# Kernel tuning notes

Measured on AMD Instinct MI355X. Metric: run time of the kernel, lower is better.

Reference implementation:

```python
import jax, jax.numpy as jnp
import numpy as np

LMAX = 2; C = 64; H = 8; D = C // H
N_NODES = 10000; N_EDGES = 160000
M = (LMAX + 1) ** 2                      # 9 spherical components
RAD_IN = 64; RAD_HID = 64
WNUM = (LMAX + 1) * C                    # per-edge CP-TP weights: one per (l, channel)
L_OF_M = jnp.array([l for l in range(LMAX + 1) for _ in range(2 * l + 1)])
LN_EPS = 1e-5


def _lin(x, W, b=None):
    # Linear over channel (last) dim; bias applied ONLY to scalar (m=0) component
    y = jnp.einsum('nmc,cd->nmd', x, W)
    if b is not None:
        y = y.at[:, 0, :].add(b)
    return y


def _cp_tp(x, sh, w_lc):
    # CP tensor product with SH: channelwise product, per-(l, channel) radial weight
    # x: [E, M, C], sh: [E, M], w_lc: [E, LMAX+1, C]
    return x * sh[:, :, None] * w_lc[:, L_OF_M, :]


def _radial(s, W1, b1, g, b, W2, off):
    h = s @ W1 + b1
    mu = h.mean(-1, keepdims=True)
    var = h.var(-1, keepdims=True)
    h = (h - mu) / jnp.sqrt(var + LN_EPS) * g + b
    h = jax.nn.silu(h)
    return (h @ W2 + off).reshape(-1, LMAX + 1, C)


def _smooth_lrelu(x, a=0.2):
    return (1 + a) / 2 * x + (1 - a) / 2 * x * (2 * jax.nn.sigmoid(x) - 1)


def _gate(x):
    c = x.shape[-1] // 2
    v = x[..., :c]
    g = jax.nn.sigmoid(x[:, 0, c:])[:, None, :]
    return jnp.concatenate([jax.nn.silu(v[:, :1, :]), v[:, 1:, :] * g], axis=1)


def _seg_softmax(a, idx, n):
    # numerically stable softmax over edges grouped by destination node
    m = jax.ops.segment_max(a, idx, num_segments=n)
    e = jnp.exp(a - m[idx])
    s = jax.ops.segment_sum(e, idx, num_segments=n)
    return e / (s[idx] + 1e-16)


def setup_inputs():
    key = jax.random.key(0)
    ks = jax.random.split(key, 16)
    def w(k, shape, fan_in):
        return jax.random.normal(k, shape, jnp.float32) / np.sqrt(fan_in)
    bound = 1.0 / np.sqrt(RAD_HID)
    return {
        'node_input': jax.random.normal(ks[0], (N_NODES, M, C), jnp.float32),
        'edge_attr': jax.random.normal(ks[1], (N_EDGES, M), jnp.float32),
        'edge_scalars': jax.random.normal(ks[2], (N_EDGES, RAD_IN), jnp.float32),
        'W_src': w(ks[3], (C, C), C), 'b_src': jnp.zeros((C,), jnp.float32),
        'W_dst': w(ks[4], (C, C), C),
        'rad_W1': w(ks[5], (RAD_IN, RAD_HID), RAD_IN),
        'rad_b1': jnp.zeros((RAD_HID,), jnp.float32),
        'rad_ln_g': jnp.ones((RAD_HID,), jnp.float32),
        'rad_ln_b': jnp.zeros((RAD_HID,), jnp.float32),
        'rad_W2': w(ks[6], (RAD_HID, WNUM), RAD_HID),
        'rad_offset': jax.random.uniform(ks[7], (WNUM,), jnp.float32, -bound, bound),
        'W_alpha': w(ks[8], (C, C), C), 'b_alpha': jnp.zeros((C,), jnp.float32),
        'alpha_dot': w(ks[9], (H, D), D),
        'W_value': w(ks[10], (C, 2 * C), C), 'b_value': jnp.zeros((2 * C,), jnp.float32),
        'W_proj': w(ks[11], (C, C), C), 'b_proj': jnp.zeros((C,), jnp.float32),
        'edge_src': jax.random.randint(ks[12], (N_EDGES,), 0, N_NODES),
        'edge_dst': jax.random.randint(ks[13], (N_EDGES,), 0, N_NODES),
        'batch': jnp.zeros((N_NODES,), jnp.int32),
    }


def reference(node_input, edge_attr, edge_scalars, W_src, b_src, W_dst,
              rad_W1, rad_b1, rad_ln_g, rad_ln_b, rad_W2, rad_offset,
              W_alpha, b_alpha, alpha_dot, W_value, b_value, W_proj, b_proj,
              edge_src, edge_dst, batch):
    # gather: per-edge merged message [E, M, C]
    msg = _lin(node_input, W_src, b_src)[edge_src] + _lin(node_input, W_dst)[edge_dst]
    # per-edge radial weights for both tensor products [E, LMAX+1, C]
    w_lc = _radial(edge_scalars, rad_W1, rad_b1, rad_ln_g, rad_ln_b, rad_W2, rad_offset)
    msg = _cp_tp(msg, edge_attr, w_lc)
    # alpha path: scalar channel only
    alpha = _lin(msg, W_alpha, b_alpha)[:, 0, :].reshape(-1, H, D)
    alpha = _smooth_lrelu(alpha)[:, None]                 # [E, 1, H, D]
    alpha = jnp.einsum('bikd,kd->bik', alpha, alpha_dot)  # [E, 1, H]
    alpha = _seg_softmax(alpha, edge_dst, N_NODES)        # dropout disabled (eval)
    # value path
    value = _gate(_lin(msg, W_value, b_value))
    value = _cp_tp(value, edge_attr, w_lc)
    value = value.reshape(N_EDGES, M, H, D)
    # scatter-aggregate to destination nodes
    out = jax.ops.segment_sum(value * alpha[:, :, :, None], edge_dst, num_segments=N_NODES)
    return _lin(out.reshape(N_NODES, M, C), W_proj, b_proj)
```

## Files before the change

kernel.cpp:

```cpp
#include <hip/hip_runtime.h>
#include <stdint.h>

#define NN 10000
#define NE 160000

struct BF16 { unsigned short v; };
typedef _Float16 h2_t __attribute__((ext_vector_type(2)));
typedef _Float16 f16x8 __attribute__((ext_vector_type(8)));
typedef float f32x4 __attribute__((ext_vector_type(4)));

__device__ __forceinline__ float cvt(float x) { return x; }
__device__ __forceinline__ float cvt(BF16 x) {
    union { unsigned int i; float f; } u; u.i = ((unsigned int)x.v) << 16; return u.f;
}
__device__ __forceinline__ unsigned short f2b_us(float f) {
    union { float f; unsigned int i; } v; v.f = f;
    unsigned int x = v.i;
    unsigned int lsb = (x >> 16) & 1u;
    x += 0x7fffu + lsb;
    return (unsigned short)(x >> 16);
}
__device__ __forceinline__ float rlane(float v, int l) {
    return __uint_as_float((unsigned int)__builtin_amdgcn_readlane(__float_as_uint(v), l));
}
__device__ __forceinline__ h2_t rlane_pk(h2_t v, int l) {
    union { h2_t h; unsigned int u; } c; c.h = v;
    c.u = (unsigned int)__builtin_amdgcn_readlane(c.u, l);
    return c.h;
}
__device__ __forceinline__ h2_t pkh2(float a, float b) {
    h2_t r; r[0] = (_Float16)a; r[1] = (_Float16)b; return r;
}
__device__ __forceinline__ float fdot2f(h2_t a, h2_t b, float c) {
#if __has_builtin(__builtin_amdgcn_fdot2)
    return __builtin_amdgcn_fdot2(a, b, c, false);
#else
    return fmaf((float)a[0], (float)b[0], fmaf((float)a[1], (float)b[1], c));
#endif
}
__device__ __forceinline__ float sigm(float x) { return 1.0f / (1.0f + __expf(-x)); }
__device__ __forceinline__ int clampi(int v, int hi) { return (unsigned)v >= (unsigned)hi ? 0 : v; }

__device__ __forceinline__ void stOut(float* p, size_t i, float v) { p[i] = v; }
__device__ __forceinline__ void stOut(unsigned short* p, size_t i, float v) { p[i] = f2b_us(v); }

__device__ __forceinline__ unsigned okey(float f) {
    unsigned b = __float_as_uint(f);
    return (b & 0x80000000u) ? ~b : (b | 0x80000000u);
}
__device__ __forceinline__ float okdec(unsigned k) {
    unsigned b = (k & 0x80000000u) ? (k ^ 0x80000000u) : ~k;
    return __uint_as_float(b);
}

__device__ __forceinline__ f16x8 ld8f16(const BF16* p) {
    uint4 v = *(const uint4*)p;
    unsigned w0 = v.x, w1 = v.y, w2 = v.z, w3 = v.w;
    f16x8 r;
    union { unsigned u; float f; } c;
    c.u = (w0 & 0xFFFFu) << 16;  r[0] = (_Float16)c.f;
    c.u = (w0 & 0xFFFF0000u);    r[1] = (_Float16)c.f;
    c.u = (w1 & 0xFFFFu) << 16;  r[2] = (_Float16)c.f;
    c.u = (w1 & 0xFFFF0000u);    r[3] = (_Float16)c.f;
    c.u = (w2 & 0xFFFFu) << 16;  r[4] = (_Float16)c.f;
    c.u = (w2 & 0xFFFF0000u);    r[5] = (_Float16)c.f;
    c.u = (w3 & 0xFFFFu) << 16;  r[6] = (_Float16)c.f;
    c.u = (w3 & 0xFFFF0000u);    r[7] = (_Float16)c.f;
    return r;
}
__device__ __forceinline__ f16x8 ld8f16(const float* p) {
    float4 a = *(const float4*)p;
    float4 b = *(const float4*)(p + 4);
    f16x8 r;
    r[0] = (_Float16)a.x; r[1] = (_Float16)a.y; r[2] = (_Float16)a.z; r[3] = (_Float16)a.w;
    r[4] = (_Float16)b.x; r[5] = (_Float16)b.y; r[6] = (_Float16)b.z; r[7] = (_Float16)b.w;
    return r;
}

__global__ void k0_zero(int* __restrict__ cnt, int* __restrict__ csr, int* __restrict__ flag,
                        float* __restrict__ nsum, unsigned* __restrict__ mseg,
                        float* __restrict__ sseg) {
    int i = blockIdx.x * blockDim.x + threadIdx.x;
    if (i == 0) *flag = 1;
    if (i < NN) cnt[i] = 0;
    if (i < NE) csr[i] = 0;
    if (i < NN * 8) { mseg[i] = 0u; sseg[i] = 0.f; }
    for (int j = i; j < NN * 576; j += gridDim.x * blockDim.x) nsum[j] = 0.f;
}

__global__ void kprobe(const unsigned short* __restrict__ x, int* __restrict__ flag) {
    int bad = 0;
    for (int i = threadIdx.x; i < 16384; i += blockDim.x) {
        unsigned e = (x[i] >> 7) & 0xFFu;
        bad += (e == 0xFFu);
    }
    if (bad > 0) atomicExch(flag, 0);
}

template<typename T>
__device__ void k1_body(const T* x, const T* Ws, const T* bs, const T* Wd,
                        _Float16* fs, _Float16* fd)
{
    int lane = threadIdx.x & 63;
    int wv = threadIdx.x >> 6;
    float ws[64], wd[64];
#pragma unroll
    for (int i = 0; i < 64; i++) { ws[i] = cvt(Ws[i * 64 + lane]); wd[i] = cvt(Wd[i * 64 + lane]); }
    float bsl = cvt(bs[lane]);
    const int ROWS = NN * 9;
    for (int r = blockIdx.x * 4 + wv; r < ROWS; r += gridDim.x * 4) {
        float xv = cvt(x[(size_t)r * 64 + lane]);
        float a0 = 0, a1 = 0, a2 = 0, a3 = 0, d0 = 0, d1 = 0, d2 = 0, d3 = 0;
#pragma unroll
        for (int i = 0; i < 64; i += 4) {
            float x0 = rlane(xv, i), x1 = rlane(xv, i + 1), x2 = rlane(xv, i + 2), x3 = rlane(xv, i + 3);
            a0 = fmaf(x0, ws[i], a0);     a1 = fmaf(x1, ws[i + 1], a1);
            a2 = fmaf(x2, ws[i + 2], a2); a3 = fmaf(x3, ws[i + 3], a3);
            d0 = fmaf(x0, wd[i], d0);     d1 = fmaf(x1, wd[i + 1], d1);
            d2 = fmaf(x2, wd[i + 2], d2); d3 = fmaf(x3, wd[i + 3], d3);
        }
        float as = a0 + a1 + a2 + a3;
        if ((r % 9) == 0) as += bsl;
        fs[(size_t)r * 64 + lane] = (_Float16)as;
        fd[(size_t)r * 64 + lane] = (_Float16)(d0 + d1 + d2 + d3);
    }
}

__global__ __launch_bounds__(256) void k1_feats(
    const void* x, const void* Ws, const void* bs, const void* Wd,
    _Float16* fs, _Float16* fd, const int* flag)
{
    if (*flag) k1_body((const BF16*)x, (const BF16*)Ws, (const BF16*)bs, (const BF16*)Wd, fs, fd);
    else       k1_body((const float*)x, (const float*)Ws, (const float*)bs, (const float*)Wd, fs, fd);
}

__global__ void k2a_count(const int* __restrict__ dst, int* __restrict__ cnt) {
    for (int e = blockIdx.x * blockDim.x + threadIdx.x; e < NE; e += gridDim.x * blockDim.x)
        atomicAdd(&cnt[clampi(dst[e], NN)], 1);
}

__global__ __launch_bounds__(1024) void k2b_scan(const int* __restrict__ cnt,
                                                 int* __restrict__ off, int* __restrict__ cur) {
    __shared__ int part[1024];
    int t = threadIdx.x;
    int base = t * 10;
    int loc[10]; int s = 0;
#pragma unroll
    for (int k = 0; k < 10; k++) { int i = base + k; int v = (i < NN) ? cnt[i] : 0; loc[k] = v; s += v; }
    part[t] = s; __syncthreads();
    for (int o = 1; o < 1024; o <<= 1) {
        int v = (t >= o) ? part[t - o] : 0;
        __syncthreads();
        part[t] += v;
        __syncthreads();
    }
    int run = (t == 0) ? 0 : part[t - 1];
#pragma unroll
    for (int k = 0; k < 10; k++) {
        int i = base + k;
        if (i < NN) { off[i] = run; cur[i] = run; run += loc[k]; }
    }
    if (t == 1023) off[NN] = part[1023];
}

__global__ void k2c_fill(const int* __restrict__ dst, int* __restrict__ cur, int* __restrict__ csr) {
    for (int e = blockIdx.x * blockDim.x + threadIdx.x; e < NE; e += gridDim.x * blockDim.x) {
        int d = clampi(dst[e], NN);
        int p = atomicAdd(&cur[d], 1);
        if ((unsigned)p < (unsigned)NE) csr[p] = e;
    }
}

template<typename T>
__device__ void k3m_body(const T* es, const T* W1, const T* b1g, const T* gg, const T* bbv,
                         const T* W2, const T* roff, _Float16* wlc,
                         _Float16 (*Yt)[200])
{
    const int lane = threadIdx.x & 63;
    const int c16 = lane & 15;
    const int kg  = lane >> 4;

    f16x8 bW1[4][2], bW2[12][2];
#pragma unroll
    for (int t = 0; t < 4; t++)
#pragma unroll
        for (int kh = 0; kh < 2; kh++) {
            f16x8 f;
#pragma unroll
            for (int j = 0; j < 8; j++) {
                int k = kh * 32 + kg * 8 + j;
                f[j] = (_Float16)cvt(W1[(size_t)k * 64 + t * 16 + c16]);
            }
            bW1[t][kh] = f;
        }
#pragma unroll
    for (int t = 0; t < 12; t++)
#pragma unroll
        for (int kh = 0; kh < 2; kh++) {
            f16x8 f;
#pragma unroll
            for (int j = 0; j < 8; j++) {
                int k = kh * 32 + kg * 8 + j;
                f[j] = (_Float16)cvt(W2[(size_t)k * 192 + t * 16 + c16]);
            }
            bW2[t][kh] = f;
        }
    float b1v[4], gv[4], bv[4], rv[12];
#pragma unroll
    for (int t = 0; t < 4; t++) {
        b1v[t] = cvt(b1g[t * 16 + c16]);
        gv[t]  = cvt(gg[t * 16 + c16]);
        bv[t]  = cvt(bbv[t * 16 + c16]);
    }
#pragma unroll
    for (int t = 0; t < 12; t++) rv[t] = cvt(roff[t * 16 + c16]);

    const int NT = NE / 16;
    for (int tile = blockIdx.x * 4 + (threadIdx.x >> 6); tile < NT; tile += gridDim.x * 4) {
        const int e0 = tile * 16;
        f16x8 a0 = ld8f16(&es[(size_t)(e0 + c16) * 64 + kg * 8]);
        f16x8 a1 = ld8f16(&es[(size_t)(e0 + c16) * 64 + 32 + kg * 8]);
        f32x4 h[4] = {{0,0,0,0},{0,0,0,0},{0,0,0,0},{0,0,0,0}};
#pragma unroll
        for (int t = 0; t < 4; t++) {
            h[t] = __builtin_amdgcn_mfma_f32_16x16x32_f16(a0, bW1[t][0], h[t], 0, 0, 0);
            h[t] = __builtin_amdgcn_mfma_f32_16x16x32_f16(a1, bW1[t][1], h[t], 0, 0, 0);
        }
#pragma unroll
        for (int r = 0; r < 4; r++) {
            float x0 = h[0][r] + b1v[0], x1 = h[1][r] + b1v[1];
            float x2 = h[2][r] + b1v[2], x3 = h[3][r] + b1v[3];
            float s = x0 + x1 + x2 + x3;
            float q = x0 * x0 + x1 * x1 + x2 * x2 + x3 * x3;
            s += __shfl_xor(s, 1, 64); q += __shfl_xor(q, 1, 64);
            s += __shfl_xor(s, 2, 64); q += __shfl_xor(q, 2, 64);
            s += __shfl_xor(s, 4, 64); q += __shfl_xor(q, 4, 64);
            s += __shfl_xor(s, 8, 64); q += __shfl_xor(q, 8, 64);
            float mu = s * (1.0f / 64.0f);
            float var = fmaxf(q * (1.0f / 64.0f) - mu * mu, 0.0f);
            float rs = rsqrtf(var + 1e-5f);
            int row = kg * 4 + r;
#pragma unroll
            for (int t = 0; t < 4; t++) {
                float xt = (t == 0) ? x0 : (t == 1) ? x1 : (t == 2) ? x2 : x3;
                float v = (xt - mu) * rs * gv[t] + bv[t];
                v = v * sigm(v);
                Yt[row][t * 16 + c16] = (_Float16)v;
            }
        }
        f16x8 a20 = *(const f16x8*)&Yt[c16][kg * 8];
        f16x8 a21 = *(const f16x8*)&Yt[c16][32 + kg * 8];
        f32x4 y[12] = {{0,0,0,0},{0,0,0,0},{0,0,0,0},{0,0,0,0},{0,0,0,0},{0,0,0,0},
                       {0,0,0,0},{0,0,0,0},{0,0,0,0},{0,0,0,0},{0,0,0,0},{0,0,0,0}};
#pragma unroll
        for (int t = 0; t < 12; t++) {
            y[t] = __builtin_amdgcn_mfma_f32_16x16x32_f16(a20, bW2[t][0], y[t], 0, 0, 0);
            y[t] = __builtin_amdgcn_mfma_f32_16x16x32_f16(a21, bW2[t][1], y[t], 0, 0, 0);
        }
#pragma unroll
        for (int t = 0; t < 12; t++)
#pragma unroll
            for (int r = 0; r < 4; r++)
                Yt[kg * 4 + r][t * 16 + c16] = (_Float16)(y[t][r] + rv[t]);
#pragma unroll
        for (int j = 0; j < 6; j++) {
            int c = lane + 64 * j;
            int row = c / 24;
            int cc = (c % 24) * 8;
            *(f16x8*)&wlc[(size_t)(e0 + row) * 192 + cc] = *(const f16x8*)&Yt[row][cc];
        }
    }
}

__global__ __launch_bounds__(256) void k3m_wlc(
    const void* es, const void* W1, const void* b1, const void* g, const void* bln,
    const void* W2, const void* roff, _Float16* wlc, const int* flag)
{
    __shared__ _Float16 Y[4][16][200];
    const int wv = threadIdx.x >> 6;
    if (*flag) k3m_body<BF16>((const BF16*)es, (const BF16*)W1, (const BF16*)b1, (const BF16*)g,
                              (const BF16*)bln, (const BF16*)W2, (const BF16*)roff, wlc, Y[wv]);
    else       k3m_body<float>((const float*)es, (const float*)W1, (const float*)b1, (const float*)g,
                               (const float*)bln, (const float*)W2, (const float*)roff, wlc, Y[wv]);
}

template<typename T>
__device__ void k4_body(const T* ea, const _Float16* fs, const _Float16* fd,
                        const _Float16* wlc, const T* Wa, const T* ba, const T* adot,
                        const int* esrc, const int* edst, float* alpha, unsigned* mseg)
{
    int lane = threadIdx.x & 63;
    int wv = threadIdx.x >> 6;
    int j2 = (lane & 31) * 2;
    h2_t wap[32];
#pragma unroll
    for (int i = 0; i < 32; i++)
        wap[i] = pkh2(cvt(Wa[(2 * i) * 64 + lane]), cvt(Wa[(2 * i + 1) * 64 + lane]));
    float bal = cvt(ba[lane]), adl = cvt(adot[lane]);
    for (int e = blockIdx.x * 4 + wv; e < NE; e += gridDim.x * 4) {
        int sn = clampi(esrc[e], NN), dn = clampi(edst[e], NN);
        h2_t fsp = *(const h2_t*)&fs[(size_t)sn * 576 + j2];
        h2_t fdp = *(const h2_t*)&fd[(size_t)dn * 576 + j2];
        h2_t wlp = *(const h2_t*)&wlc[(size_t)e * 192 + j2];
        float ea0 = cvt(ea[(size_t)e * 9]);
        float m0a = ((float)fsp[0] + (float)fdp[0]) * ea0 * (float)wlp[0];
        float m0b = ((float)fsp[1] + (float)fdp[1]) * ea0 * (float)wlp[1];
        h2_t m0p = pkh2(m0a, m0b);
        float a0 = bal, a1 = 0, a2 = 0, a3 = 0;
#pragma unroll
        for (int i = 0; i < 32; i += 4) {
            a0 = fdot2f(rlane_pk(m0p, i),     wap[i],     a0);
            a1 = fdot2f(rlane_pk(m0p, i + 1), wap[i + 1], a1);
            a2 = fdot2f(rlane_pk(m0p, i + 2), wap[i + 2], a2);
            a3 = fdot2f(rlane_pk(m0p, i + 3), wap[i + 3], a3);
        }
        float aw = a0 + a1 + a2 + a3;
        float f = aw * (0.2f + 0.8f * sigm(aw));
        float p = f * adl;
        p += __shfl_xor(p, 1, 64);
        p += __shfl_xor(p, 2, 64);
        p += __shfl_xor(p, 4, 64);
        if ((lane & 7) == 0) {
            alpha[(size_t)e * 8 + (lane >> 3)] = p;
            atomicMax(&mseg[dn * 8 + (lane >> 3)], okey(p));
        }
    }
}

__global__ __launch_bounds__(256) void k4_alpha(
    const void* ea, const _Float16* fs, const _Float16* fd, const _Float16* wlc,
    const void* Wa, const void* ba, const void* adot,
    const int* esrc, const int* edst, float* alpha, unsigned* mseg, const int* flag)
{
    if (*flag) k4_body((const BF16*)ea, fs, fd, wlc, (const BF16*)Wa, (const BF16*)ba,
                       (const BF16*)adot, esrc, edst, alpha, mseg);
    else       k4_body((const float*)ea, fs, fd, wlc, (const float*)Wa, (const float*)ba,
                       (const float*)adot, esrc, edst, alpha, mseg);
}

__global__ void k5b_expsum(const int* __restrict__ edst, const unsigned* __restrict__ mseg,
                           float* __restrict__ alpha, float* __restrict__ sseg) {
    int t = blockIdx.x * blockDim.x + threadIdx.x;
    if (t >= NE * 8) return;
    int e = t >> 3, h = t & 7;
    int dn = clampi(edst[e], NN);
    float m = okdec(mseg[dn * 8 + h]);
    float ex = __expf(alpha[t] - m);
    alpha[t] = ex;
    unsafeAtomicAdd(&sseg[dn * 8 + h], ex);
}

template<typename T>
__device__ void k6m_body(const int* off, const int* csr, const int* esrc,
                         const T* ea, const _Float16* fs, const _Float16* fd,
                         const _Float16* wlc, const T* Wv, const T* bv,
                         const float* alpha, const float* sseg, float* nsum,
                         _Float16 (*wlS)[16][72], float (*mtS)[20])
{
    const int lane = threadIdx.x & 63;
    const int wvid = threadIdx.x >> 6;
    const int c16 = lane & 15;
    const int kg  = lane >> 4;

    for (int gw = blockIdx.x * 4 + wvid; gw < NN * 2; gw += gridDim.x * 4) {
        const int n = gw >> 1;
        const int half = gw & 1;
        const int b = off[n], e_end = off[n + 1];
        if (b >= e_end) continue;

        f16x8 bfV[2][2], bfG[2][2];
        float bvv[2], bgv[2];
        int colg[2], hh[2];
        float invs[2];
#pragma unroll
        for (int t = 0; t < 2; t++) {
            colg[t] = (half * 2 + t) * 16 + c16;
            hh[t] = colg[t] >> 3;
            invs[t] = 1.0f / (sseg[n * 8 + hh[t]] + 1e-16f);
#pragma unroll
            for (int kh = 0; kh < 2; kh++) {
                f16x8 b8v, b8g;
#pragma unroll
                for (int j = 0; j < 8; j++) {
                    int k = kh * 32 + kg * 8 + j;
                    b8v[j] = (_Float16)cvt(Wv[(size_t)k * 128 + colg[t]]);
                    b8g[j] = (_Float16)cvt(Wv[(size_t)k * 128 + 64 + colg[t]]);
                }
                bfV[t][kh] = b8v; bfG[t][kh] = b8g;
            }
            bvv[t] = cvt(bv[colg[t]]);
            bgv[t] = cvt(bv[64 + colg[t]]);
        }

        const size_t fdb = (size_t)n * 576;
        const size_t nbase = (size_t)n * 576;

        for (int p0 = b; p0 < e_end; p0 += 16) {
            int pA = p0 + c16; if (pA >= e_end) pA = e_end - 1;
            const int eA = clampi(csr[pA], NE);
            const int snA = clampi(esrc[eA], NN);
            const size_t fsb = (size_t)snA * 576;
            const size_t wlb = (size_t)eA * 192;

#pragma unroll
            for (int l = 0; l < 3; l++)
#pragma unroll
                for (int kh = 0; kh < 2; kh++)
                    *(f16x8*)&wlS[l][c16][kh * 32 + kg * 8] =
                        *(const f16x8*)&wlc[wlb + (size_t)l * 64 + kh * 32 + kg * 8];
            float eao[9];
#pragma unroll
            for (int m = 0; m < 9; m++) eao[m] = cvt(ea[(size_t)eA * 9 + m]);
            if (kg == 0) {
#pragma unroll
                for (int m = 0; m < 9; m++) mtS[c16][m] = eao[m];
            }
            mtS[c16][10 + kg * 2]     = alpha[(size_t)eA * 8 + kg * 2];
            mtS[c16][10 + kg * 2 + 1] = alpha[(size_t)eA * 8 + kg * 2 + 1];

            float awm[2][4];
#pragma unroll
            for (int r = 0; r < 4; r++) {
                int row = kg * 4 + r;
                float vm = (p0 + row < e_end) ? 1.f : 0.f;
#pragma unroll
                for (int t = 0; t < 2; t++)
                    awm[t][r] = mtS[row][10 + hh[t]] * invs[t] * vm;
            }

            float gtv[2][4];
            {
                f16x8 a0, a1;
                {
                    f16x8 w0 = *(const f16x8*)&wlS[0][c16][kg * 8];
                    f16x8 w1 = *(const f16x8*)&wlS[0][c16][32 + kg * 8];
                    f16x8 fd0 = *(const f16x8*)&fd[fdb + kg * 8];
                    f16x8 fd1 = *(const f16x8*)&fd[fdb + 32 + kg * 8];
                    f16x8 fs0 = *(const f16x8*)&fs[fsb + kg * 8];
                    f16x8 fs1 = *(const f16x8*)&fs[fsb + 32 + kg * 8];
                    _Float16 eh = (_Float16)eao[0];
                    f16x8 ev;
#pragma unroll
                    for (int j = 0; j < 8; j++) ev[j] = eh;
                    a0 = (fs0 + fd0) * ev * w0;
                    a1 = (fs1 + fd1) * ev * w1;
                }
                f32x4 d[2] = {{0,0,0,0},{0,0,0,0}};
                f32x4 g[2] = {{0,0,0,0},{0,0,0,0}};
#pragma unroll
                for (int t = 0; t < 2; t++) {
                    d[t] = __builtin_amdgcn_mfma_f32_16x16x32_f16(a0, bfV[t][0], d[t], 0, 0, 0);
                    d[t] = __builtin_amdgcn_mfma_f32_16x16x32_f16(a1, bfV[t][1], d[t], 0, 0, 0);
                    g[t] = __builtin_amdgcn_mfma_f32_16x16x32_f16(a0, bfG[t][0], g[t], 0, 0, 0);
                    g[t] = __builtin_amdgcn_mfma_f32_16x16x32_f16(a1, bfG[t][1], g[t], 0, 0, 0);
                }
#pragma unroll
                for (int t = 0; t < 2; t++) {
                    float ps = 0.f;
#pragma unroll
                    for (int r = 0; r < 4; r++) {
                        int row = kg * 4 + r;
                        gtv[t][r] = sigm(g[t][r] + bgv[t]);
                        float v = d[t][r] + bvv[t];
                        float f = v * sigm(v);
                        float wlv = (float)wlS[0][row][colg[t]];
                        float eam = mtS[row][0];
                        ps = fmaf(f * (eam * wlv), awm[t][r], ps);
                    }
                    ps += __shfl_xor(ps, 16, 64);
                    ps += __shfl_xor(ps, 32, 64);
                    if (kg == 0) unsafeAtomicAdd(&nsum[nbase + colg[t]], ps);
                }
            }
#pragma unroll 2
            for (int m = 1; m < 9; m++) {
                const int l = (m < 4) ? 1 : 2;
                f16x8 a0, a1;
                {
                    const size_t mo = (size_t)m * 64;
                    f16x8 w0 = *(const f16x8*)&wlS[l][c16][kg * 8];
                    f16x8 w1 = *(const f16x8*)&wlS[l][c16][32 + kg * 8];
                    f16x8 fd0 = *(const f16x8*)&fd[fdb + mo + kg * 8];
                    f16x8 fd1 = *(const f16x8*)&fd[fdb + mo + 32 + kg * 8];
                    f16x8 fs0 = *(const f16x8*)&fs[fsb + mo + kg * 8];
                    f16x8 fs1 = *(const f16x8*)&fs[fsb + mo + 32 + kg * 8];
                    _Float16 eh = (_Float16)eao[m];
                    f16x8 ev;
#pragma unroll
                    for (int j = 0; j < 8; j++) ev[j] = eh;
                    a0 = (fs0 + fd0) * ev * w0;
                    a1 = (fs1 + fd1) * ev * w1;
                }
                f32x4 d[2] = {{0,0,0,0},{0,0,0,0}};
#pragma unroll
                for (int t = 0; t < 2; t++) {
                    d[t] = __builtin_amdgcn_mfma_f32_16x16x32_f16(a0, bfV[t][0], d[t], 0, 0, 0);
                    d[t] = __builtin_amdgcn_mfma_f32_16x16x32_f16(a1, bfV[t][1], d[t], 0, 0, 0);
                }
#pragma unroll
                for (int t = 0; t < 2; t++) {
                    float ps = 0.f;
#pragma unroll
                    for (int r = 0; r < 4; r++) {
                        int row = kg * 4 + r;
                        float f = d[t][r] * gtv[t][r];
                        float wlv = (float)wlS[l][row][colg[t]];
                        float eam = mtS[row][m];
                        ps = fmaf(f * (eam * wlv), awm[t][r], ps);
                    }
                    ps += __shfl_xor(ps, 16, 64);
                    ps += __shfl_xor(ps, 32, 64);
                    if (kg == 0) unsafeAtomicAdd(&nsum[nbase + (size_t)m * 64 + colg[t]], ps);
                }
            }
        }
    }
}

__global__ __launch_bounds__(256) void k6m_fused(
    const int* off, const int* csr, const int* esrc,
    const void* ea, const _Float16* fs, const _Float16* fd, const _Float16* wlc,
    const void* Wv, const void* bv,
    const float* alpha, const float* sseg, float* nsum, const int* flag)
{
    __shared__ _Float16 shwl[4][3][16][72];
    __shared__ float    shmt[4][16][20];
    const int wvid = threadIdx.x >> 6;
    if (*flag) k6m_body<BF16>(off, csr, esrc, (const BF16*)ea, fs, fd, wlc,
                              (const BF16*)Wv, (const BF16*)bv, alpha, sseg, nsum,
                              shwl[wvid], shmt[wvid]);
    else       k6m_body<float>(off, csr, esrc, (const float*)ea, fs, fd, wlc,
                               (const float*)Wv, (const float*)bv, alpha, sseg, nsum,
                               shwl[wvid], shmt[wvid]);
}

template<typename T, typename OT>
__device__ void k7_body(const float* nsum, const T* Wp, const T* bp, OT* out)
{
    int lane = threadIdx.x & 63;
    int wv = threadIdx.x >> 6;
    float wp[64];
#pragma unroll
    for (int i = 0; i < 64; i++) wp[i] = cvt(Wp[i * 64 + lane]);
    float bpl = cvt(bp[lane]);
    const int ROWS = NN * 9;
    for (int r = blockIdx.x * 4 + wv; r < ROWS; r += gridDim.x * 4) {
        float xv = nsum[(size_t)r * 64 + lane];
        float o0 = 0, o1 = 0, o2 = 0, o3 = 0;
#pragma unroll
        for (int i = 0; i < 64; i += 4) {
            o0 = fmaf(rlane(xv, i), wp[i], o0);
            o1 = fmaf(rlane(xv, i + 1), wp[i + 1], o1);
            o2 = fmaf(rlane(xv, i + 2), wp[i + 2], o2);
            o3 = fmaf(rlane(xv, i + 3), wp[i + 3], o3);
        }
        float o = o0 + o1 + o2 + o3;
        if ((r % 9) == 0) o += bpl;
        stOut(out, (size_t)r * 64 + lane, o);
    }
}

__global__ __launch_bounds__(256) void k7_proj(
    const float* nsum, const void* Wp, const void* bp, void* out, const int* flag)
{
    if (*flag) k7_body<BF16, unsigned short>(nsum, (const BF16*)Wp, (const BF16*)bp, (unsigned short*)out);
    else       k7_body<float, float>(nsum, (const float*)Wp, (const float*)bp, (float*)out);
}

extern "C" void kernel_launch(void* const* d_in, const int* in_sizes, int n_in,
                              void* d_out, int out_size, void* d_ws, size_t ws_size,
                              hipStream_t stream) {
    const void* node_input = d_in[0];
    const void* edge_attr  = d_in[1];
    const void* edge_scal  = d_in[2];
    const void* W_src      = d_in[3];
    const void* b_src      = d_in[4];
    const void* W_dst      = d_in[5];
    const void* rad_W1     = d_in[6];
    const void* rad_b1     = d_in[7];
    const void* rad_ln_g   = d_in[8];
    const void* rad_ln_b   = d_in[9];
    const void* rad_W2     = d_in[10];
    const void* rad_off    = d_in[11];
    const void* W_alpha    = d_in[12];
    const void* b_alpha    = d_in[13];
    const void* alpha_dot  = d_in[14];
    const void* W_value    = d_in[15];
    const void* b_value    = d_in[16];
    const void* W_proj     = d_in[17];
    const void* b_proj     = d_in[18];
    const int* edge_src    = (const int*)d_in[19];
    const int* edge_dst    = (const int*)d_in[20];

    char* ws = (char*)d_ws;
    size_t ofs = 0;
    auto alloc = [&](size_t bytes) -> char* {
        char* r = ws + ofs;
        ofs = (ofs + bytes + 255) & ~(size_t)255;
        return r;
    };

    int* flag       = (int*)alloc(256);
    int* cnt        = (int*)alloc((size_t)NN * 4);
    int* offs       = (int*)alloc((size_t)(NN + 16) * 4);
    int* cur        = (int*)alloc((size_t)NN * 4);
    int* csr        = (int*)alloc((size_t)NE * 4);
    unsigned* mseg  = (unsigned*)alloc((size_t)NN * 8 * 4);
    float* sseg     = (float*)alloc((size_t)NN * 8 * 4);
    float* alpha    = (float*)alloc((size_t)NE * 8 * 4);
    _Float16* fs    = (_Float16*)alloc((size_t)NN * 576 * 2);
    _Float16* fd    = (_Float16*)alloc((size_t)NN * 576 * 2);
    _Float16* wlc   = (_Float16*)alloc((size_t)NE * 192 * 2);
    float* nsum32   = (float*)alloc((size_t)NN * 576 * 4);

    k0_zero<<<dim3(625), dim3(256), 0, stream>>>(cnt, csr, flag, nsum32, mseg, sseg);
    kprobe<<<dim3(1), dim3(256), 0, stream>>>((const unsigned short*)node_input, flag);
    k1_feats<<<dim3(2048), dim3(256), 0, stream>>>(node_input, W_src, b_src, W_dst, fs, fd, flag);
    k2a_count<<<dim3(512), dim3(256), 0, stream>>>(edge_dst, cnt);
    k2b_scan<<<dim3(1), dim3(1024), 0, stream>>>(cnt, offs, cur);
    k2c_fill<<<dim3(512), dim3(256), 0, stream>>>(edge_dst, cur, csr);
    k3m_wlc<<<dim3(512), dim3(256), 0, stream>>>(edge_scal, rad_W1, rad_b1, rad_ln_g, rad_ln_b,
                                                 rad_W2, rad_off, wlc, flag);
    k4_alpha<<<dim3(2048), dim3(256), 0, stream>>>(edge_attr, fs, fd, wlc, W_alpha, b_alpha,
                                                   alpha_dot, edge_src, edge_dst, alpha, mseg, flag);
    k5b_expsum<<<dim3(5000), dim3(256), 0, stream>>>(edge_dst, mseg, alpha, sseg);
    k6m_fused<<<dim3(5000), dim3(256), 0, stream>>>(offs, csr, edge_src, edge_attr, fs, fd, wlc,
                                                    W_value, b_value, alpha, sseg, nsum32, flag);
    k7_proj<<<dim3(2048), dim3(256), 0, stream>>>(nsum32, W_proj, b_proj, d_out, flag);
}
```

Before: 543.4 us.

## Fuse softmax exp-sum, value aggregation and output projection into one node kernel

Removes the separate exp/sum kernel and the final projection kernel. Each node's wave now computes the softmax denominator by walking its CSR edges, accumulates the per-node messages in registers instead of issuing global float atomics into a zeroed buffer, and applies W_proj with MFMA from shared memory before writing the output directly. This drops the nsum and sseg buffers, their zeroing and the atomic traffic, at the cost of a second pass over alpha per node and an fp16 rounding of the aggregated sums before projection. The kernel also changes from a grid-stride loop to exactly one node-half per wave and adds a block barrier.

```diff
diff --git a/kernel.cpp b/kernel.cpp
--- a/kernel.cpp
+++ b/kernel.cpp
@@ -78,14 +78,12 @@
 }
 
 __global__ void k0_zero(int* __restrict__ cnt, int* __restrict__ csr, int* __restrict__ flag,
-                        float* __restrict__ nsum, unsigned* __restrict__ mseg,
-                        float* __restrict__ sseg) {
+                        unsigned* __restrict__ mseg) {
     int i = blockIdx.x * blockDim.x + threadIdx.x;
     if (i == 0) *flag = 1;
     if (i < NN) cnt[i] = 0;
     if (i < NE) csr[i] = 0;
-    if (i < NN * 8) { mseg[i] = 0u; sseg[i] = 0.f; }
-    for (int j = i; j < NN * 576; j += gridDim.x * blockDim.x) nsum[j] = 0.f;
+    if (i < NN * 8) mseg[i] = 0u;
 }
 
 __global__ void kprobe(const unsigned short* __restrict__ x, int* __restrict__ flag) {
@@ -338,233 +336,237 @@
                        (const float*)adot, esrc, edst, alpha, mseg);
 }
 
-__global__ void k5b_expsum(const int* __restrict__ edst, const unsigned* __restrict__ mseg,
-                           float* __restrict__ alpha, float* __restrict__ sseg) {
-    int t = blockIdx.x * blockDim.x + threadIdx.x;
-    if (t >= NE * 8) return;
-    int e = t >> 3, h = t & 7;
-    int dn = clampi(edst[e], NN);
-    float m = okdec(mseg[dn * 8 + h]);
-    float ex = __expf(alpha[t] - m);
-    alpha[t] = ex;
-    unsafeAtomicAdd(&sseg[dn * 8 + h], ex);
-}
-
-template<typename T>
-__device__ void k6m_body(const int* off, const int* csr, const int* esrc,
+template<typename T, typename OT>
+__device__ void k6f_body(const int* off, const int* csr, const int* esrc,
                          const T* ea, const _Float16* fs, const _Float16* fd,
                          const _Float16* wlc, const T* Wv, const T* bv,
-                         const float* alpha, const float* sseg, float* nsum,
-                         _Float16 (*wlS)[16][72], float (*mtS)[20])
+                         const T* Wp, const T* bp,
+                         const float* alpha, const unsigned* mseg, OT* out,
+                         _Float16 (*wlS)[16][72], float (*mtS)[20],
+                         _Float16 (*nsS)[72])
 {
     const int lane = threadIdx.x & 63;
-    const int wvid = threadIdx.x >> 6;
     const int c16 = lane & 15;
     const int kg  = lane >> 4;
-
-    for (int gw = blockIdx.x * 4 + wvid; gw < NN * 2; gw += gridDim.x * 4) {
-        const int n = gw >> 1;
-        const int half = gw & 1;
-        const int b = off[n], e_end = off[n + 1];
-        if (b >= e_end) continue;
-
-        f16x8 bfV[2][2], bfG[2][2];
-        float bvv[2], bgv[2];
-        int colg[2], hh[2];
-        float invs[2];
+    const int gw  = blockIdx.x * 4 + (threadIdx.x >> 6);
+    const int n = gw >> 1;
+    const int half = gw & 1;
+    const int b = off[n], e_end = off[n + 1];
+
+    f16x8 bfV[2][2], bfG[2][2], bfP[2][2];
+    float bvv[2], bgv[2], bpv[2];
+    int colg[2], hh[2];
+#pragma unroll
+    for (int t = 0; t < 2; t++) {
+        colg[t] = (half * 2 + t) * 16 + c16;
+        hh[t] = colg[t] >> 3;
+#pragma unroll
+        for (int kh = 0; kh < 2; kh++) {
+            f16x8 b8v, b8g, b8p;
+#pragma unroll
+            for (int j = 0; j < 8; j++) {
+                int k = kh * 32 + kg * 8 + j;
+                b8v[j] = (_Float16)cvt(Wv[(size_t)k * 128 + colg[t]]);
+                b8g[j] = (_Float16)cvt(Wv[(size_t)k * 128 + 64 + colg[t]]);
+                b8p[j] = (_Float16)cvt(Wp[(size_t)k * 64 + colg[t]]);
+            }
+            bfV[t][kh] = b8v; bfG[t][kh] = b8g; bfP[t][kh] = b8p;
+        }
+        bvv[t] = cvt(bv[colg[t]]);
+        bgv[t] = cvt(bv[64 + colg[t]]);
+        bpv[t] = cvt(bp[colg[t]]);
+    }
+
+    float mhA = okdec(mseg[n * 8 + kg * 2]);
+    float mhB = okdec(mseg[n * 8 + kg * 2 + 1]);
+    float sl = 0.f;
+    {
+        float ml = okdec(mseg[n * 8 + (lane & 7)]);
+        for (int p = b + (lane >> 3); p < e_end; p += 8) {
+            int e = clampi(csr[p], NE);
+            sl += __expf(alpha[(size_t)e * 8 + (lane & 7)] - ml);
+        }
+        sl += __shfl_xor(sl, 8, 64);
+        sl += __shfl_xor(sl, 16, 64);
+        sl += __shfl_xor(sl, 32, 64);
+    }
+    float invs[2];
+    invs[0] = 1.0f / (__shfl(sl, hh[0], 8) + 1e-16f);
+    invs[1] = 1.0f / (__shfl(sl, hh[1], 8) + 1e-16f);
+
+    float accT[9][2];
+#pragma unroll
+    for (int m = 0; m < 9; m++) { accT[m][0] = 0.f; accT[m][1] = 0.f; }
+
+    const size_t fdb = (size_t)n * 576;
+
+    for (int p0 = b; p0 < e_end; p0 += 16) {
+        int pA = p0 + c16; if (pA >= e_end) pA = e_end - 1;
+        const int eA = clampi(csr[pA], NE);
+        const int snA = clampi(esrc[eA], NN);
+        const size_t fsb = (size_t)snA * 576;
+        const size_t wlb = (size_t)eA * 192;
+
+#pragma unroll
+        for (int l = 0; l < 3; l++)
+#pragma unroll
+            for (int kh = 0; kh < 2; kh++)
+                *(f16x8*)&wlS[l][c16][kh * 32 + kg * 8] =
+                    *(const f16x8*)&wlc[wlb + (size_t)l * 64 + kh * 32 + kg * 8];
+        float eao[9];
+#pragma unroll
+        for (int m = 0; m < 9; m++) eao[m] = cvt(ea[(size_t)eA * 9 + m]);
+        if (kg == 0) {
+#pragma unroll
+            for (int m = 0; m < 9; m++) mtS[c16][m] = eao[m];
+        }
+        mtS[c16][10 + kg * 2]     = __expf(alpha[(size_t)eA * 8 + kg * 2]     - mhA);
+        mtS[c16][10 + kg * 2 + 1] = __expf(alpha[(size_t)eA * 8 + kg * 2 + 1] - mhB);
+
+        float awm[2][4];
+#pragma unroll
+        for (int r = 0; r < 4; r++) {
+            int row = kg * 4 + r;
+            float vm = (p0 + row < e_end) ? 1.f : 0.f;
+#pragma unroll
+            for (int t = 0; t < 2; t++)
+                awm[t][r] = mtS[row][10 + hh[t]] * invs[t] * vm;
+        }
+
+        float gtv[2][4];
+        {
+            f16x8 a0, a1;
+            {
+                f16x8 w0 = *(const f16x8*)&wlS[0][c16][kg * 8];
+                f16x8 w1 = *(const f16x8*)&wlS[0][c16][32 + kg * 8];
+                f16x8 fd0 = *(const f16x8*)&fd[fdb + kg * 8];
+                f16x8 fd1 = *(const f16x8*)&fd[fdb + 32 + kg * 8];
+                f16x8 fs0 = *(const f16x8*)&fs[fsb + kg * 8];
+                f16x8 fs1 = *(const f16x8*)&fs[fsb + 32 + kg * 8];
+                _Float16 eh = (_Float16)eao[0];
+                f16x8 ev;
+#pragma unroll
+                for (int j = 0; j < 8; j++) ev[j] = eh;
+                a0 = (fs0 + fd0) * ev * w0;
+                a1 = (fs1 + fd1) * ev * w1;
+            }
+            f32x4 d[2] = {{0,0,0,0},{0,0,0,0}};
+            f32x4 g[2] = {{0,0,0,0},{0,0,0,0}};
+#pragma unroll
+            for (int t = 0; t < 2; t++) {
+                d[t] = __builtin_amdgcn_mfma_f32_16x16x32_f16(a0, bfV[t][0], d[t], 0, 0, 0);
+                d[t] = __builtin_amdgcn_mfma_f32_16x16x32_f16(a1, bfV[t][1], d[t], 0, 0, 0);
+                g[t] = __builtin_amdgcn_mfma_f32_16x16x32_f16(a0, bfG[t][0], g[t], 0, 0, 0);
+                g[t] = __builtin_amdgcn_mfma_f32_16x16x32_f16(a1, bfG[t][1], g[t], 0, 0, 0);
+            }
+#pragma unroll
+            for (int t = 0; t < 2; t++) {
+                float ps = 0.f;
+#pragma unroll
+                for (int r = 0; r < 4; r++) {
+                    int row = kg * 4 + r;
+                    gtv[t][r] = sigm(g[t][r] + bgv[t]);
+                    float v = d[t][r] + bvv[t];
+                    float f = v * sigm(v);
+                    float wlv = (float)wlS[0][row][colg[t]];
+                    float eam = mtS[row][0];
+                    ps = fmaf(f * (eam * wlv), awm[t][r], ps);
+                }
+                accT[0][t] += ps;
+            }
+        }
+#pragma unroll
+        for (int m = 1; m < 9; m++) {
+            const int l = (m < 4) ? 1 : 2;
+            f16x8 a0, a1;
+            {
+                const size_t mo = (size_t)m * 64;
+                f16x8 w0 = *(const f16x8*)&wlS[l][c16][kg * 8];
+                f16x8 w1 = *(const f16x8*)&wlS[l][c16][32 + kg * 8];
+                f16x8 fd0 = *(const f16x8*)&fd[fdb + mo + kg * 8];
+                f16x8 fd1 = *(const f16x8*)&fd[fdb + mo + 32 + kg * 8];
+                f16x8 fs0 = *(const f16x8*)&fs[fsb + mo + kg * 8];
+                f16x8 fs1 = *(const f16x8*)&fs[fsb + mo + 32 + kg * 8];
+                _Float16 eh = (_Float16)eao[m];
+                f16x8 ev;
+#pragma unroll
+                for (int j = 0; j < 8; j++) ev[j] = eh;
+                a0 = (fs0 + fd0) * ev * w0;
+                a1 = (fs1 + fd1) * ev * w1;
+            }
+            f32x4 d[2] = {{0,0,0,0},{0,0,0,0}};
+#pragma unroll
+            for (int t = 0; t < 2; t++) {
+                d[t] = __builtin_amdgcn_mfma_f32_16x16x32_f16(a0, bfV[t][0], d[t], 0, 0, 0);
+                d[t] = __builtin_amdgcn_mfma_f32_16x16x32_f16(a1, bfV[t][1], d[t], 0, 0, 0);
+            }
+#pragma unroll
+            for (int t = 0; t < 2; t++) {
+                float ps = 0.f;
+#pragma unroll
+                for (int r = 0; r < 4; r++) {
+                    int row = kg * 4 + r;
+                    float f = d[t][r] * gtv[t][r];
+                    float wlv = (float)wlS[l][row][colg[t]];
+                    float eam = mtS[row][m];
+                    ps = fmaf(f * (eam * wlv), awm[t][r], ps);
+                }
+                accT[m][t] += ps;
+            }
+        }
+    }
+
+#pragma unroll
+    for (int m = 0; m < 9; m++)
 #pragma unroll
         for (int t = 0; t < 2; t++) {
-            colg[t] = (half * 2 + t) * 16 + c16;
-            hh[t] = colg[t] >> 3;
-            invs[t] = 1.0f / (sseg[n * 8 + hh[t]] + 1e-16f);
-#pragma unroll
-            for (int kh = 0; kh < 2; kh++) {
-                f16x8 b8v, b8g;
-#pragma unroll
-                for (int j = 0; j < 8; j++) {
-                    int k = kh * 32 + kg * 8 + j;
-                    b8v[j] = (_Float16)cvt(Wv[(size_t)k * 128 + colg[t]]);
-                    b8g[j] = (_Float16)cvt(Wv[(size_t)k * 128 + 64 + colg[t]]);
-                }
-                bfV[t][kh] = b8v; bfG[t][kh] = b8g;
-            }
-            bvv[t] = cvt(bv[colg[t]]);
-            bgv[t] = cvt(bv[64 + colg[t]]);
-        }
-
-        const size_t fdb = (size_t)n * 576;
-        const size_t nbase = (size_t)n * 576;
-
-        for (int p0 = b; p0 < e_end; p0 += 16) {
-            int pA = p0 + c16; if (pA >= e_end) pA = e_end - 1;
-            const int eA = clampi(csr[pA], NE);
-            const int snA = clampi(esrc[eA], NN);
-            const size_t fsb = (size_t)snA * 576;
-            const size_t wlb = (size_t)eA * 192;
-
-#pragma unroll
-            for (int l = 0; l < 3; l++)
-#pragma unroll
-                for (int kh = 0; kh < 2; kh++)
-                    *(f16x8*)&wlS[l][c16][kh * 32 + kg * 8] =
-                        *(const f16x8*)&wlc[wlb + (size_t)l * 64 + kh * 32 + kg * 8];
-            float eao[9];
-#pragma unroll
-            for (int m = 0; m < 9; m++) eao[m] = cvt(ea[(size_t)eA * 9 + m]);
-            if (kg == 0) {
-#pragma unroll
-                for (int m = 0; m < 9; m++) mtS[c16][m] = eao[m];
-            }
-            mtS[c16][10 + kg * 2]     = alpha[(size_t)eA * 8 + kg * 2];
-            mtS[c16][10 + kg * 2 + 1] = alpha[(size_t)eA * 8 + kg * 2 + 1];
-
-            float awm[2][4];
-#pragma unroll
-            for (int r = 0; r < 4; r++) {
-                int row = kg * 4 + r;
-                float vm = (p0 + row < e_end) ? 1.f : 0.f;
-#pragma unroll
-                for (int t = 0; t < 2; t++)
-                    awm[t][r] = mtS[row][10 + hh[t]] * invs[t] * vm;
-            }
-
-            float gtv[2][4];
-            {
-                f16x8 a0, a1;
-                {
-                    f16x8 w0 = *(const f16x8*)&wlS[0][c16][kg * 8];
-                    f16x8 w1 = *(const f16x8*)&wlS[0][c16][32 + kg * 8];
-                    f16x8 fd0 = *(const f16x8*)&fd[fdb + kg * 8];
-                    f16x8 fd1 = *(const f16x8*)&fd[fdb + 32 + kg * 8];
-                    f16x8 fs0 = *(const f16x8*)&fs[fsb + kg * 8];
-                    f16x8 fs1 = *(const f16x8*)&fs[fsb + 32 + kg * 8];
-                    _Float16 eh = (_Float16)eao[0];
-                    f16x8 ev;
-#pragma unroll
-                    for (int j = 0; j < 8; j++) ev[j] = eh;
-                    a0 = (fs0 + fd0) * ev * w0;
-                    a1 = (fs1 + fd1) * ev * w1;
-                }
-                f32x4 d[2] = {{0,0,0,0},{0,0,0,0}};
-                f32x4 g[2] = {{0,0,0,0},{0,0,0,0}};
-#pragma unroll
-                for (int t = 0; t < 2; t++) {
-                    d[t] = __builtin_amdgcn_mfma_f32_16x16x32_f16(a0, bfV[t][0], d[t], 0, 0, 0);
-                    d[t] = __builtin_amdgcn_mfma_f32_16x16x32_f16(a1, bfV[t][1], d[t], 0, 0, 0);
-                    g[t] = __builtin_amdgcn_mfma_f32_16x16x32_f16(a0, bfG[t][0], g[t], 0, 0, 0);
-                    g[t] = __builtin_amdgcn_mfma_f32_16x16x32_f16(a1, bfG[t][1], g[t], 0, 0, 0);
-                }
-#pragma unroll
-                for (int t = 0; t < 2; t++) {
-                    float ps = 0.f;
-#pragma unroll
-                    for (int r = 0; r < 4; r++) {
-                        int row = kg * 4 + r;
-                        gtv[t][r] = sigm(g[t][r] + bgv[t]);
-                        float v = d[t][r] + bvv[t];
-                        float f = v * sigm(v);
-                        float wlv = (float)wlS[0][row][colg[t]];
-                        float eam = mtS[row][0];
-                        ps = fmaf(f * (eam * wlv), awm[t][r], ps);
-                    }
-                    ps += __shfl_xor(ps, 16, 64);
-                    ps += __shfl_xor(ps, 32, 64);
-                    if (kg == 0) unsafeAtomicAdd(&nsum[nbase + colg[t]], ps);
-                }
-            }
-#pragma unroll 2
-            for (int m = 1; m < 9; m++) {
-                const int l = (m < 4) ? 1 : 2;
-                f16x8 a0, a1;
-                {
-                    const size_t mo = (size_t)m * 64;
-                    f16x8 w0 = *(const f16x8*)&wlS[l][c16][kg * 8];
-                    f16x8 w1 = *(const f16x8*)&wlS[l][c16][32 + kg * 8];
-                    f16x8 fd0 = *(const f16x8*)&fd[fdb + mo + kg * 8];
-                    f16x8 fd1 = *(const f16x8*)&fd[fdb + mo + 32 + kg * 8];
-                    f16x8 fs0 = *(const f16x8*)&fs[fsb + mo + kg * 8];
-                    f16x8 fs1 = *(const f16x8*)&fs[fsb + mo + 32 + kg * 8];
-                    _Float16 eh = (_Float16)eao[m];
-                    f16x8 ev;
-#pragma unroll
-                    for (int j = 0; j < 8; j++) ev[j] = eh;
-                    a0 = (fs0 + fd0) * ev * w0;
-                    a1 = (fs1 + fd1) * ev * w1;
-                }
-                f32x4 d[2] = {{0,0,0,0},{0,0,0,0}};
-#pragma unroll
-                for (int t = 0; t < 2; t++) {
-                    d[t] = __builtin_amdgcn_mfma_f32_16x16x32_f16(a0, bfV[t][0], d[t], 0, 0, 0);
-                    d[t] = __builtin_amdgcn_mfma_f32_16x16x32_f16(a1, bfV[t][1], d[t], 0, 0, 0);
-                }
-#pragma unroll
-                for (int t = 0; t < 2; t++) {
-                    float ps = 0.f;
-#pragma unroll
-                    for (int r = 0; r < 4; r++) {
-                        int row = kg * 4 + r;
-                        float f = d[t][r] * gtv[t][r];
-                        float wlv = (float)wlS[l][row][colg[t]];
-                        float eam = mtS[row][m];
-                        ps = fmaf(f * (eam * wlv), awm[t][r], ps);
-                    }
-                    ps += __shfl_xor(ps, 16, 64);
-                    ps += __shfl_xor(ps, 32, 64);
-                    if (kg == 0) unsafeAtomicAdd(&nsum[nbase + (size_t)m * 64 + colg[t]], ps);
-                }
-            }
-        }
-    }
-}
-
-__global__ __launch_bounds__(256) void k6m_fused(
+            float ps = accT[m][t];
+            ps += __shfl_xor(ps, 16, 64);
+            ps += __shfl_xor(ps, 32, 64);
+            if (kg == 0) nsS[m][colg[t]] = (_Float16)ps;
+        }
+    __syncthreads();
+
+    f16x8 aP0 = *(const f16x8*)&nsS[c16][kg * 8];
+    f16x8 aP1 = *(const f16x8*)&nsS[c16][32 + kg * 8];
+    f32x4 dP[2] = {{0,0,0,0},{0,0,0,0}};
+#pragma unroll
+    for (int t = 0; t < 2; t++) {
+        dP[t] = __builtin_amdgcn_mfma_f32_16x16x32_f16(aP0, bfP[t][0], dP[t], 0, 0, 0);
+        dP[t] = __builtin_amdgcn_mfma_f32_16x16x32_f16(aP1, bfP[t][1], dP[t], 0, 0, 0);
+    }
+#pragma unroll
+    for (int t = 0; t < 2; t++)
+#pragma unroll
+        for (int r = 0; r < 4; r++) {
+            int m = kg * 4 + r;
+            if (m < 9) {
+                float o = dP[t][r] + ((m == 0) ? bpv[t] : 0.f);
+                stOut(out, ((size_t)n * 9 + m) * 64 + colg[t], o);
+            }
+        }
+}
+
+__global__ __launch_bounds__(256) void k6f_fused(
     const int* off, const int* csr, const int* esrc,
     const void* ea, const _Float16* fs, const _Float16* fd, const _Float16* wlc,
-    const void* Wv, const void* bv,
-    const float* alpha, const float* sseg, float* nsum, const int* flag)
+    const void* Wv, const void* bv, const void* Wp, const void* bp,
+    const float* alpha, const unsigned* mseg, void* out, const int* flag)
 {
     __shared__ _Float16 shwl[4][3][16][72];
     __shared__ float    shmt[4][16][20];
+    __shared__ _Float16 shns[2][16][72];
+    for (int i = threadIdx.x; i < 2 * 16 * 72; i += 256) ((_Float16*)shns)[i] = (_Float16)0.f;
+    __syncthreads();
     const int wvid = threadIdx.x >> 6;
-    if (*flag) k6m_body<BF16>(off, csr, esrc, (const BF16*)ea, fs, fd, wlc,
-                              (const BF16*)Wv, (const BF16*)bv, alpha, sseg, nsum,
-                              shwl[wvid], shmt[wvid]);
-    else       k6m_body<float>(off, csr, esrc, (const float*)ea, fs, fd, wlc,
-                               (const float*)Wv, (const float*)bv, alpha, sseg, nsum,
-                               shwl[wvid], shmt[wvid]);
-}
-
-template<typename T, typename OT>
-__device__ void k7_body(const float* nsum, const T* Wp, const T* bp, OT* out)
-{
-    int lane = threadIdx.x & 63;
-    int wv = threadIdx.x >> 6;
-    float wp[64];
-#pragma unroll
-    for (int i = 0; i < 64; i++) wp[i] = cvt(Wp[i * 64 + lane]);
-    float bpl = cvt(bp[lane]);
-    const int ROWS = NN * 9;
-    for (int r = blockIdx.x * 4 + wv; r < ROWS; r += gridDim.x * 4) {
-        float xv = nsum[(size_t)r * 64 + lane];
-        float o0 = 0, o1 = 0, o2 = 0, o3 = 0;
-#pragma unroll
-        for (int i = 0; i < 64; i += 4) {
-            o0 = fmaf(rlane(xv, i), wp[i], o0);
-            o1 = fmaf(rlane(xv, i + 1), wp[i + 1], o1);
-            o2 = fmaf(rlane(xv, i + 2), wp[i + 2], o2);
-            o3 = fmaf(rlane(xv, i + 3), wp[i + 3], o3);
-        }
-        float o = o0 + o1 + o2 + o3;
-        if ((r % 9) == 0) o += bpl;
-        stOut(out, (size_t)r * 64 + lane, o);
-    }
-}
-
-__global__ __launch_bounds__(256) void k7_proj(
-    const float* nsum, const void* Wp, const void* bp, void* out, const int* flag)
-{
-    if (*flag) k7_body<BF16, unsigned short>(nsum, (const BF16*)Wp, (const BF16*)bp, (unsigned short*)out);
-    else       k7_body<float, float>(nsum, (const float*)Wp, (const float*)bp, (float*)out);
+    if (*flag) k6f_body<BF16, unsigned short>(off, csr, esrc, (const BF16*)ea, fs, fd, wlc,
+                              (const BF16*)Wv, (const BF16*)bv, (const BF16*)Wp, (const BF16*)bp,
+                              alpha, mseg, (unsigned short*)out,
+                              shwl[wvid], shmt[wvid], shns[wvid >> 1]);
+    else       k6f_body<float, float>(off, csr, esrc, (const float*)ea, fs, fd, wlc,
+                              (const float*)Wv, (const float*)bv, (const float*)Wp, (const float*)bp,
+                              alpha, mseg, (float*)out,
+                              shwl[wvid], shmt[wvid], shns[wvid >> 1]);
 }
 
 extern "C" void kernel_launch(void* const* d_in, const int* in_sizes, int n_in,
@@ -606,14 +608,12 @@
     int* cur        = (int*)alloc((size_t)NN * 4);
     int* csr        = (int*)alloc((size_t)NE * 4);
     unsigned* mseg  = (unsigned*)alloc((size_t)NN * 8 * 4);
-    float* sseg     = (float*)alloc((size_t)NN * 8 * 4);
     float* alpha    = (float*)alloc((size_t)NE * 8 * 4);
     _Float16* fs    = (_Float16*)alloc((size_t)NN * 576 * 2);
     _Float16* fd    = (_Float16*)alloc((size_t)NN * 576 * 2);
     _Float16* wlc   = (_Float16*)alloc((size_t)NE * 192 * 2);
-    float* nsum32   = (float*)alloc((size_t)NN * 576 * 4);
-
-    k0_zero<<<dim3(625), dim3(256), 0, stream>>>(cnt, csr, flag, nsum32, mseg, sseg);
+
+    k0_zero<<<dim3(625), dim3(256), 0, stream>>>(cnt, csr, flag, mseg);
     kprobe<<<dim3(1), dim3(256), 0, stream>>>((const unsigned short*)node_input, flag);
     k1_feats<<<dim3(2048), dim3(256), 0, stream>>>(node_input, W_src, b_src, W_dst, fs, fd, flag);
     k2a_count<<<dim3(512), dim3(256), 0, stream>>>(edge_dst, cnt);
@@ -623,8 +623,7 @@
                                                  rad_W2, rad_off, wlc, flag);
     k4_alpha<<<dim3(2048), dim3(256), 0, stream>>>(edge_attr, fs, fd, wlc, W_alpha, b_alpha,
                                                    alpha_dot, edge_src, edge_dst, alpha, mseg, flag);
-    k5b_expsum<<<dim3(5000), dim3(256), 0, stream>>>(edge_dst, mseg, alpha, sseg);
-    k6m_fused<<<dim3(5000), dim3(256), 0, stream>>>(offs, csr, edge_src, edge_attr, fs, fd, wlc,
-                                                    W_value, b_value, alpha, sseg, nsum32, flag);
-    k7_proj<<<dim3(2048), dim3(256), 0, stream>>>(nsum32, W_proj, b_proj, d_out, flag);
-}
+    k6f_fused<<<dim3(5000), dim3(256), 0, stream>>>(offs, csr, edge_src, edge_attr, fs, fd, wlc,
+                                                    W_value, b_value, W_proj, b_proj,
+                                                    alpha, mseg, d_out, flag);
+}
```

Result: slower. 647.6 us (+19.2%).
